# Performance work log

Hardware: AMD Instinct MI355X
Metric: run time of the kernel (lower is better)

The kernel has to match this reference:

```python
import jax, jax.numpy as jnp
import numpy as np

B, K, D = 512, 36, 1024
N_KERNELS = 4
OUT_DIM = 1024
OUT_PER_KERNEL = OUT_DIM // N_KERNELS  # 256


def setup_inputs() -> dict:
    key = jax.random.key(0)
    k1, k2, k3, k4, k5 = jax.random.split(key, 5)
    neighbourhood_features = jax.random.normal(k1, (B, K, D), dtype=jnp.float32)
    region_relation_weights = jax.random.uniform(k2, (B, K, K), dtype=jnp.float32)
    # Gaussian mixture params: init uniform(0, 1) as in init_parameters()
    mean_relation = jax.random.uniform(k3, (N_KERNELS,), dtype=jnp.float32)
    precision_relation = jax.random.uniform(k4, (N_KERNELS,), dtype=jnp.float32)
    # Per-kernel Linear weights (bias=False), torch default init U(-1/sqrt(D), 1/sqrt(D))
    bound = 1.0 / np.sqrt(D)
    W = jax.random.uniform(k5, (N_KERNELS, OUT_PER_KERNEL, D), dtype=jnp.float32,
                           minval=-bound, maxval=bound)
    return {
        "neighbourhood_features": neighbourhood_features,
        "region_relation_weights": region_relation_weights,
        "mean_relation": mean_relation,
        "precision_relation": precision_relation,
        "W": W,
    }


def reference(neighbourhood_features, region_relation_weights, mean_relation,
              precision_relation, W):
    b, k, d = neighbourhood_features.shape
    # Gaussian mixture edge weights, normalized over kernels: [B,K,K,n_kernels]
    diff = (region_relation_weights[..., None] - mean_relation) ** 2
    w = jnp.exp(-0.5 * diff / (1e-14 + precision_relation ** 2))
    w = w / jnp.sum(w, axis=-1, keepdims=True)
    # Original repeats feat[b,i] over the neighbour axis j, so
    # bmm(w^T, repeated_feat)[b,i,k,:] == (sum_j w[b,i,j,k]) * feat[b,i,:].
    # Exploit that linearity instead of materializing the [B,K,K,D] repeat.
    ws = jnp.sum(w, axis=2)  # [B,K,n_kernels]
    weighted = ws[..., None] * neighbourhood_features[:, :, None, :]  # [B,K,n,D]
    # Per-kernel linear (stacked): [B,K,n_kernels,out_per_kernel]
    out = jnp.einsum('bknd,nod->bkno', weighted, W)
    # Concatenate kernel outputs -> [B,K,out_feat_dim]
    return out.reshape(b, k, -1)
```

## Files before the change

### kernel.cpp

```cpp
#include <hip/hip_runtime.h>
#include <stdint.h>

#define BB   512
#define KNB  36
#define DD   1024
#define MM   (BB*KNB)
#define NN   1024
#define NKER 4

typedef float  f32x4  __attribute__((ext_vector_type(4)));
typedef __bf16 bf16x8 __attribute__((ext_vector_type(8)));
typedef unsigned short u16;
typedef unsigned int   u32;

__device__ __forceinline__ u16 f2bf(float f) {
    u32 u = __float_as_uint(f);
    u32 r = (u + 0x7fffu + ((u >> 16) & 1u)) >> 16;
    return (u16)r;
}

__device__ __forceinline__ void gld16(const void* g, void* l) {
    __builtin_amdgcn_global_load_lds(
        (const __attribute__((address_space(1))) u32*)g,
        (__attribute__((address_space(3))) u32*)l,
        16, 0, 0);
}

__device__ __forceinline__ bf16x8 cvt8(f32x4 lo, f32x4 hi) {
    bf16x8 r;
    r[0] = (__bf16)lo.x; r[1] = (__bf16)lo.y; r[2] = (__bf16)lo.z; r[3] = (__bf16)lo.w;
    r[4] = (__bf16)hi.x; r[5] = (__bf16)hi.y; r[6] = (__bf16)hi.z; r[7] = (__bf16)hi.w;
    return r;
}

#define WS_BLOCKS 72
#define CAST_BLOCKS 512
__global__ void prep_kernel(const float* __restrict__ rrw,
                            const float* __restrict__ mean,
                            const float* __restrict__ prec,
                            float* __restrict__ wsT,
                            const float* __restrict__ W,
                            u16* __restrict__ Wbf) {
    if (blockIdx.x < WS_BLOCKS) {
        int id = blockIdx.x * 256 + threadIdx.x;
        float m0 = mean[0], m1 = mean[1], m2 = mean[2], m3 = mean[3];
        float i0 = 1.0f / (1e-14f + prec[0] * prec[0]);
        float i1 = 1.0f / (1e-14f + prec[1] * prec[1]);
        float i2 = 1.0f / (1e-14f + prec[2] * prec[2]);
        float i3 = 1.0f / (1e-14f + prec[3] * prec[3]);
        const float* p = rrw + (size_t)id * KNB;
        float a0 = 0.f, a1 = 0.f, a2 = 0.f, a3 = 0.f;
        for (int j = 0; j < KNB; ++j) {
            float x = p[j];
            float d0 = x - m0, d1 = x - m1, d2 = x - m2, d3 = x - m3;
            float e0 = expf(-0.5f * d0 * d0 * i0);
            float e1 = expf(-0.5f * d1 * d1 * i1);
            float e2 = expf(-0.5f * d2 * d2 * i2);
            float e3 = expf(-0.5f * d3 * d3 * i3);
            float inv = 1.0f / (e0 + e1 + e2 + e3);
            a0 += e0 * inv; a1 += e1 * inv; a2 += e2 * inv; a3 += e3 * inv;
        }
        wsT[0 * MM + id] = a0;
        wsT[1 * MM + id] = a1;
        wsT[2 * MM + id] = a2;
        wsT[3 * MM + id] = a3;
    } else {
        int i = (blockIdx.x - WS_BLOCKS) * 256 + threadIdx.x;
        const f32x4* p = (const f32x4*)(W + (size_t)i * 8);
        f32x4 v0 = p[0], v1 = p[1];
        union { u16 us[8]; uint4 u4; } pk;
        pk.us[0] = f2bf(v0.x); pk.us[1] = f2bf(v0.y);
        pk.us[2] = f2bf(v0.z); pk.us[3] = f2bf(v0.w);
        pk.us[4] = f2bf(v1.x); pk.us[5] = f2bf(v1.y);
        pk.us[6] = f2bf(v1.z); pk.us[7] = f2bf(v1.w);
        *((uint4*)(Wbf + (size_t)i * 8)) = pk.u4;
    }
}

#define BM 128
#define BN 128
#define BK 64
#define KTILES (DD / BK)

__global__ __launch_bounds__(256, 3) void gemm_kernel(
        const float* __restrict__ A,
        const u16* __restrict__ Bm,
        const float* __restrict__ wsT,
        float* __restrict__ out) {
    __shared__ __align__(16) u16 As[BM * BK];
    __shared__ __align__(16) u16 Bs[BN * BK];

    const int tid = threadIdx.x;
    const int bid   = blockIdx.x;
    const int xcd   = bid & 7;
    const int local = bid >> 3;
    const int by    = xcd * 18 + (local >> 3);
    const int bx    = local & 7;
    const int rowBase = by * BM;
    const int colBase = bx * BN;
    const int lane = tid & 63;
    const int w    = tid >> 6;
    const int wr   = w >> 1;
    const int wc   = w & 1;
    const int fr   = lane & 15;
    const int fq   = lane >> 4;

    f32x4 acc[4][4];
#pragma unroll
    for (int m = 0; m < 4; ++m)
#pragma unroll
        for (int n = 0; n < 4; ++n)
            acc[m][n] = (f32x4)0.0f;

    const int ar0 = tid >> 3;
    const int aj  = tid & 7;

    for (int kt = 0; kt < KTILES; ++kt) {
        f32x4 ra[4][2];
#pragma unroll
        for (int i = 0; i < 4; ++i) {
            const float* src = A + (size_t)(rowBase + i * 32 + ar0) * DD + kt * BK + aj * 8;
            ra[i][0] = *(const f32x4*)src;
            ra[i][1] = *(const f32x4*)(src + 4);
        }

        if (kt) __syncthreads();

#pragma unroll
        for (int i = 0; i < 4; ++i) {
            int id4 = i * 256 + tid;
            int r = id4 >> 3;
            int j = id4 & 7;
            int srcc = (j ^ (r & 7)) * 8;
            gld16(Bm + (size_t)(colBase + r) * DD + kt * BK + srcc, &Bs[id4 * 8]);
        }

#pragma unroll
        for (int i = 0; i < 4; ++i) {
            int r = i * 32 + ar0;
            int jj = aj ^ (r & 7);
            *(bf16x8*)&As[r * BK + jj * 8] = cvt8(ra[i][0], ra[i][1]);
        }

        __syncthreads();

#pragma unroll
        for (int kk = 0; kk < 2; ++kk) {
            bf16x8 af[4], bfv[4];
#pragma unroll
            for (int m = 0; m < 4; ++m) {
                int r = wr * 64 + m * 16 + fr;
                int s = r & 7;
                int g = kk * 4 + fq;
                af[m] = ((const bf16x8*)&As[r * BK])[g ^ s];
            }
#pragma unroll
            for (int n = 0; n < 4; ++n) {
                int r = wc * 64 + n * 16 + fr;
                int s = r & 7;
                int g = kk * 4 + fq;
                bfv[n] = ((const bf16x8*)&Bs[r * BK])[g ^ s];
            }
#pragma unroll
            for (int m = 0; m < 4; ++m)
#pragma unroll
                for (int n = 0; n < 4; ++n)
                    acc[m][n] = __builtin_amdgcn_mfma_f32_16x16x32_bf16(
                        af[m], bfv[n], acc[m][n], 0, 0, 0);
        }
    }

    const int kn = bx >> 1;
#pragma unroll
    for (int m = 0; m < 4; ++m) {
        int r0 = rowBase + wr * 64 + m * 16 + fq * 4;
        f32x4 s = *(const f32x4*)&wsT[(size_t)kn * MM + r0];
#pragma unroll
        for (int n = 0; n < 4; ++n) {
            int c = colBase + wc * 64 + n * 16 + fr;
            float* o = out + (size_t)r0 * NN + c;
            o[0 * NN] = acc[m][n][0] * s[0];
            o[1 * NN] = acc[m][n][1] * s[1];
            o[2 * NN] = acc[m][n][2] * s[2];
            o[3 * NN] = acc[m][n][3] * s[3];
        }
    }
}

extern "C" void kernel_launch(void* const* d_in, const int* in_sizes, int n_in,
                              void* d_out, int out_size, void* d_ws, size_t ws_size,
                              hipStream_t stream) {
    const float* feat = (const float*)d_in[0];
    const float* rrw  = (const float*)d_in[1];
    const float* mean = (const float*)d_in[2];
    const float* prec = (const float*)d_in[3];
    const float* W    = (const float*)d_in[4];
    float* out = (float*)d_out;

    char* ws = (char*)d_ws;
    float* wsT = (float*)ws;
    u16*   Wbf = (u16*)(ws + 294912);

    prep_kernel<<<dim3(WS_BLOCKS + CAST_BLOCKS), dim3(256), 0, stream>>>(
        rrw, mean, prec, wsT, W, Wbf);
    gemm_kernel<<<dim3((MM / BM) * (NN / BN)), dim3(256), 0, stream>>>(feat, Wbf, wsT, out);
}
```

Baseline: 74.13 us.

## Double-buffer LDS tiles to overlap global loads with MFMA compute

Adds a second LDS buffer for the A and B tiles so the next K tile's global loads (fp32 A into registers, bf16 B via direct-to-LDS) are issued before computing on the current tile. The A conversion and store go to the other buffer after compute, which leaves one barrier per iteration. The aim is to hide global memory latency behind MFMA work. In exchange, LDS per block doubles to 64KB and the launch bound drops from 3 to 2 blocks per CU, which lowers occupancy.

New measurement: 107.7 us. 1.45x slower.

```diff
diff --git a/kernel.cpp b/kernel.cpp
--- a/kernel.cpp
+++ b/kernel.cpp
@@ -82,13 +82,40 @@
 #define BK 64
 #define KTILES (DD / BK)
 
-__global__ __launch_bounds__(256, 3) void gemm_kernel(
+__device__ __forceinline__ void compute_tile(
+        const u16* as, const u16* bs, f32x4 (&acc)[4][4],
+        int wr, int wc, int fr, int fq) {
+#pragma unroll
+    for (int kk = 0; kk < 2; ++kk) {
+        bf16x8 af[4], bfv[4];
+#pragma unroll
+        for (int m = 0; m < 4; ++m) {
+            int r = wr * 64 + m * 16 + fr;
+            int g = kk * 4 + fq;
+            af[m] = ((const bf16x8*)&as[r * BK])[g ^ (r & 7)];
+        }
+#pragma unroll
+        for (int n = 0; n < 4; ++n) {
+            int r = wc * 64 + n * 16 + fr;
+            int g = kk * 4 + fq;
+            bfv[n] = ((const bf16x8*)&bs[r * BK])[g ^ (r & 7)];
+        }
+#pragma unroll
+        for (int m = 0; m < 4; ++m)
+#pragma unroll
+            for (int n = 0; n < 4; ++n)
+                acc[m][n] = __builtin_amdgcn_mfma_f32_16x16x32_bf16(
+                    af[m], bfv[n], acc[m][n], 0, 0, 0);
+    }
+}
+
+__global__ __launch_bounds__(256, 2) void gemm_kernel(
         const float* __restrict__ A,
         const u16* __restrict__ Bm,
         const float* __restrict__ wsT,
         float* __restrict__ out) {
-    __shared__ __align__(16) u16 As[BM * BK];
-    __shared__ __align__(16) u16 Bs[BN * BK];
+    __shared__ __align__(16) u16 As[2][BM * BK];
+    __shared__ __align__(16) u16 Bs[2][BN * BK];
 
     const int tid = threadIdx.x;
     const int bid   = blockIdx.x;
@@ -115,60 +142,52 @@
     const int ar0 = tid >> 3;
     const int aj  = tid & 7;
 
-    for (int kt = 0; kt < KTILES; ++kt) {
-        f32x4 ra[4][2];
+    f32x4 ra[4][2];
+
+#pragma unroll
+    for (int i = 0; i < 4; ++i) {
+        const float* src = A + (size_t)(rowBase + i * 32 + ar0) * DD + aj * 8;
+        ra[i][0] = *(const f32x4*)src;
+        ra[i][1] = *(const f32x4*)(src + 4);
+    }
+#pragma unroll
+    for (int i = 0; i < 4; ++i) {
+        int id4 = i * 256 + tid;
+        int r = id4 >> 3, j = id4 & 7;
+        gld16(Bm + (size_t)(colBase + r) * DD + (j ^ (r & 7)) * 8, &Bs[0][id4 * 8]);
+    }
+#pragma unroll
+    for (int i = 0; i < 4; ++i) {
+        int r = i * 32 + ar0;
+        *(bf16x8*)&As[0][r * BK + (aj ^ (r & 7)) * 8] = cvt8(ra[i][0], ra[i][1]);
+    }
+    __syncthreads();
+
+    for (int kt = 0; kt < KTILES - 1; ++kt) {
+        const int cur = kt & 1, nxt = cur ^ 1;
 #pragma unroll
         for (int i = 0; i < 4; ++i) {
-            const float* src = A + (size_t)(rowBase + i * 32 + ar0) * DD + kt * BK + aj * 8;
+            const float* src = A + (size_t)(rowBase + i * 32 + ar0) * DD
+                                 + (kt + 1) * BK + aj * 8;
             ra[i][0] = *(const f32x4*)src;
             ra[i][1] = *(const f32x4*)(src + 4);
         }
-
-        if (kt) __syncthreads();
-
 #pragma unroll
         for (int i = 0; i < 4; ++i) {
             int id4 = i * 256 + tid;
-            int r = id4 >> 3;
-            int j = id4 & 7;
-            int srcc = (j ^ (r & 7)) * 8;
-            gld16(Bm + (size_t)(colBase + r) * DD + kt * BK + srcc, &Bs[id4 * 8]);
-        }
-
+            int r = id4 >> 3, j = id4 & 7;
+            gld16(Bm + (size_t)(colBase + r) * DD + (kt + 1) * BK + (j ^ (r & 7)) * 8,
+                  &Bs[nxt][id4 * 8]);
+        }
+        compute_tile(As[cur], Bs[cur], acc, wr, wc, fr, fq);
 #pragma unroll
         for (int i = 0; i < 4; ++i) {
             int r = i * 32 + ar0;
-            int jj = aj ^ (r & 7);
-            *(bf16x8*)&As[r * BK + jj * 8] = cvt8(ra[i][0], ra[i][1]);
-        }
-
+            *(bf16x8*)&As[nxt][r * BK + (aj ^ (r & 7)) * 8] = cvt8(ra[i][0], ra[i][1]);
+        }
         __syncthreads();
-
-#pragma unroll
-        for (int kk = 0; kk < 2; ++kk) {
-            bf16x8 af[4], bfv[4];
-#pragma unroll
-            for (int m = 0; m < 4; ++m) {
-                int r = wr * 64 + m * 16 + fr;
-                int s = r & 7;
-                int g = kk * 4 + fq;
-                af[m] = ((const bf16x8*)&As[r * BK])[g ^ s];
-            }
-#pragma unroll
-            for (int n = 0; n < 4; ++n) {
-                int r = wc * 64 + n * 16 + fr;
-                int s = r & 7;
-                int g = kk * 4 + fq;
-                bfv[n] = ((const bf16x8*)&Bs[r * BK])[g ^ s];
-            }
-#pragma unroll
-            for (int m = 0; m < 4; ++m)
-#pragma unroll
-                for (int n = 0; n < 4; ++n)
-                    acc[m][n] = __builtin_amdgcn_mfma_f32_16x16x32_bf16(
-                        af[m], bfv[n], acc[m][n], 0, 0, 0);
-        }
-    }
+    }
+    compute_tile(As[1], Bs[1], acc, wr, wc, fr, fq);
 
     const int kn = bx >> 1;
 #pragma unroll
```

## Pre-cast activations to swizzled bf16 in prep kernel and load both operands via LDS DMA

Applied to the files above, without the earlier changes.

The prep kernel now also converts the fp32 feature matrix to bf16, writing it with the XOR swizzle already applied, and the weights are cast with the same pre-swizzle. The GEMM then loads both A and B tiles straight into LDS with global_load_lds and no longer does per-tile register loads and conversions. Launch bounds are raised to 4 blocks per CU. The cost is an extra full pass over the 75MB fp32 activation: it is read once and written as bf16, then read again by the GEMM, in place of the in-GEMM conversion.

New measurement: 73.88 us. Within noise of the previous version (-0.3%).

```diff
diff --git a/kernel.cpp b/kernel.cpp
--- a/kernel.cpp
+++ b/kernel.cpp
@@ -6,7 +6,6 @@
 #define DD   1024
 #define MM   (BB*KNB)
 #define NN   1024
-#define NKER 4
 
 typedef float  f32x4  __attribute__((ext_vector_type(4)));
 typedef __bf16 bf16x8 __attribute__((ext_vector_type(8)));
@@ -26,23 +25,35 @@
         16, 0, 0);
 }
 
-__device__ __forceinline__ bf16x8 cvt8(f32x4 lo, f32x4 hi) {
-    bf16x8 r;
-    r[0] = (__bf16)lo.x; r[1] = (__bf16)lo.y; r[2] = (__bf16)lo.z; r[3] = (__bf16)lo.w;
-    r[4] = (__bf16)hi.x; r[5] = (__bf16)hi.y; r[6] = (__bf16)hi.z; r[7] = (__bf16)hi.w;
-    return r;
+__device__ __forceinline__ void cast_chunk_swz(const float* __restrict__ in,
+                                               u16* __restrict__ out,
+                                               long long c, int r) {
+    long long src = (c & ~7LL) | ((c & 7) ^ (r & 7));
+    const f32x4* p = (const f32x4*)(in + src * 8);
+    f32x4 v0 = p[0], v1 = p[1];
+    union { u16 us[8]; uint4 u4; } pk;
+    pk.us[0] = f2bf(v0.x); pk.us[1] = f2bf(v0.y);
+    pk.us[2] = f2bf(v0.z); pk.us[3] = f2bf(v0.w);
+    pk.us[4] = f2bf(v1.x); pk.us[5] = f2bf(v1.y);
+    pk.us[6] = f2bf(v1.z); pk.us[7] = f2bf(v1.w);
+    *((uint4*)(out + c * 8)) = pk.u4;
 }
 
-#define WS_BLOCKS 72
-#define CAST_BLOCKS 512
+#define WS_BLOCKS   72
+#define CW_BLOCKS   512
+#define CA_BLOCKS   1152
+#define CA_THREADS  (CA_BLOCKS * 256)
 __global__ void prep_kernel(const float* __restrict__ rrw,
                             const float* __restrict__ mean,
                             const float* __restrict__ prec,
                             float* __restrict__ wsT,
                             const float* __restrict__ W,
-                            u16* __restrict__ Wbf) {
-    if (blockIdx.x < WS_BLOCKS) {
-        int id = blockIdx.x * 256 + threadIdx.x;
+                            u16* __restrict__ Wbf,
+                            const float* __restrict__ A,
+                            u16* __restrict__ Abf) {
+    const int blk = blockIdx.x;
+    if (blk < WS_BLOCKS) {
+        int id = blk * 256 + threadIdx.x;
         float m0 = mean[0], m1 = mean[1], m2 = mean[2], m3 = mean[3];
         float i0 = 1.0f / (1e-14f + prec[0] * prec[0]);
         float i1 = 1.0f / (1e-14f + prec[1] * prec[1]);
@@ -64,16 +75,18 @@
         wsT[1 * MM + id] = a1;
         wsT[2 * MM + id] = a2;
         wsT[3 * MM + id] = a3;
+    } else if (blk < WS_BLOCKS + CW_BLOCKS) {
+        long long c = (long long)(blk - WS_BLOCKS) * 256 + threadIdx.x;
+        int r = (int)(c >> 7);
+        cast_chunk_swz(W, Wbf, c, r);
     } else {
-        int i = (blockIdx.x - WS_BLOCKS) * 256 + threadIdx.x;
-        const f32x4* p = (const f32x4*)(W + (size_t)i * 8);
-        f32x4 v0 = p[0], v1 = p[1];
-        union { u16 us[8]; uint4 u4; } pk;
-        pk.us[0] = f2bf(v0.x); pk.us[1] = f2bf(v0.y);
-        pk.us[2] = f2bf(v0.z); pk.us[3] = f2bf(v0.w);
-        pk.us[4] = f2bf(v1.x); pk.us[5] = f2bf(v1.y);
-        pk.us[6] = f2bf(v1.z); pk.us[7] = f2bf(v1.w);
-        *((uint4*)(Wbf + (size_t)i * 8)) = pk.u4;
+        long long t = (long long)(blk - WS_BLOCKS - CW_BLOCKS) * 256 + threadIdx.x;
+#pragma unroll
+        for (int k = 0; k < 8; ++k) {
+            long long c = t + (long long)k * CA_THREADS;
+            int r = (int)(c >> 7);
+            cast_chunk_swz(A, Abf, c, r);
+        }
     }
 }
 
@@ -82,8 +95,8 @@
 #define BK 64
 #define KTILES (DD / BK)
 
-__global__ __launch_bounds__(256, 3) void gemm_kernel(
-        const float* __restrict__ A,
+__global__ __launch_bounds__(256, 4) void gemm_kernel(
+        const u16* __restrict__ A,
         const u16* __restrict__ Bm,
         const float* __restrict__ wsT,
         float* __restrict__ out) {
@@ -112,36 +125,16 @@
         for (int n = 0; n < 4; ++n)
             acc[m][n] = (f32x4)0.0f;
 
-    const int ar0 = tid >> 3;
-    const int aj  = tid & 7;
+    const u16* aptr = A  + (size_t)(rowBase + (tid >> 3)) * DD + (tid & 7) * 8;
+    const u16* bptr = Bm + (size_t)(colBase + (tid >> 3)) * DD + (tid & 7) * 8;
 
     for (int kt = 0; kt < KTILES; ++kt) {
-        f32x4 ra[4][2];
+        if (kt) __syncthreads();
 #pragma unroll
         for (int i = 0; i < 4; ++i) {
-            const float* src = A + (size_t)(rowBase + i * 32 + ar0) * DD + kt * BK + aj * 8;
-            ra[i][0] = *(const f32x4*)src;
-            ra[i][1] = *(const f32x4*)(src + 4);
+            gld16(aptr + (size_t)i * 32 * DD + kt * BK, &As[(i * 256 + tid) * 8]);
+            gld16(bptr + (size_t)i * 32 * DD + kt * BK, &Bs[(i * 256 + tid) * 8]);
         }
-
-        if (kt) __syncthreads();
-
-#pragma unroll
-        for (int i = 0; i < 4; ++i) {
-            int id4 = i * 256 + tid;
-            int r = id4 >> 3;
-            int j = id4 & 7;
-            int srcc = (j ^ (r & 7)) * 8;
-            gld16(Bm + (size_t)(colBase + r) * DD + kt * BK + srcc, &Bs[id4 * 8]);
-        }
-
-#pragma unroll
-        for (int i = 0; i < 4; ++i) {
-            int r = i * 32 + ar0;
-            int jj = aj ^ (r & 7);
-            *(bf16x8*)&As[r * BK + jj * 8] = cvt8(ra[i][0], ra[i][1]);
-        }
-
         __syncthreads();
 
 #pragma unroll
@@ -150,16 +143,14 @@
 #pragma unroll
             for (int m = 0; m < 4; ++m) {
                 int r = wr * 64 + m * 16 + fr;
-                int s = r & 7;
                 int g = kk * 4 + fq;
-                af[m] = ((const bf16x8*)&As[r * BK])[g ^ s];
+                af[m] = ((const bf16x8*)&As[r * BK])[g ^ (r & 7)];
             }
 #pragma unroll
             for (int n = 0; n < 4; ++n) {
                 int r = wc * 64 + n * 16 + fr;
-                int s = r & 7;
                 int g = kk * 4 + fq;
-                bfv[n] = ((const bf16x8*)&Bs[r * BK])[g ^ s];
+                bfv[n] = ((const bf16x8*)&Bs[r * BK])[g ^ (r & 7)];
             }
 #pragma unroll
             for (int m = 0; m < 4; ++m)
@@ -200,8 +191,9 @@
     char* ws = (char*)d_ws;
     float* wsT = (float*)ws;
     u16*   Wbf = (u16*)(ws + 294912);
+    u16*   Abf = (u16*)(ws + 294912 + 2097152);
 
-    prep_kernel<<<dim3(WS_BLOCKS + CAST_BLOCKS), dim3(256), 0, stream>>>(
-        rrw, mean, prec, wsT, W, Wbf);
-    gemm_kernel<<<dim3((MM / BM) * (NN / BN)), dim3(256), 0, stream>>>(feat, Wbf, wsT, out);
+    prep_kernel<<<dim3(WS_BLOCKS + CW_BLOCKS + CA_BLOCKS), dim3(256), 0, stream>>>(
+        rrw, mean, prec, wsT, W, Wbf, feat, Abf);
+    gemm_kernel<<<dim3((MM / BM) * (NN / BN)), dim3(256), 0, stream>>>(Abf, Wbf, wsT, out);
 }
```
